# Kernel tuning notes

Hardware: AMD Instinct MI355X
Metric: run time of the kernel (lower is better)

## Reference

```python
import jax, jax.numpy as jnp
import numpy as np

N_HEADS = 16
D_HEAD = 64
THETA = 10000.0


def _rope_tables(S, dh, dtype):
    inv_freq = 1.0 / (THETA ** (jnp.arange(0, dh, 2, dtype=jnp.float32) / dh))  # [dh/2]
    ang = jnp.arange(S, dtype=jnp.float32)[:, None] * inv_freq[None, :]  # [S, dh/2]
    return jnp.cos(ang).astype(dtype), jnp.sin(ang).astype(dtype)


def _apply_rope(t, cos, sin):
    # t: [B,S,H,dh]; interleaved complex pairs (even=real, odd=imag)
    B, S, H, dh = t.shape
    tr = t.reshape(B, S, H, dh // 2, 2)
    a, b = tr[..., 0], tr[..., 1]
    c = cos[None, :, None, :]
    s = sin[None, :, None, :]
    ra = a * c - b * s
    rb = a * s + b * c
    return jnp.stack([ra, rb], axis=-1).reshape(B, S, H, dh)


def setup_inputs() -> dict:
    key = jax.random.key(0)
    ks = jax.random.split(key, 5)
    B, S, D = 2, 2048, 1024
    x = jax.random.normal(ks[0], (B, S, D), dtype=jnp.float32)
    scale = 1.0 / np.sqrt(D)
    wq = jax.random.normal(ks[1], (D, D), dtype=jnp.float32) * scale
    wk = jax.random.normal(ks[2], (D, D), dtype=jnp.float32) * scale
    wv = jax.random.normal(ks[3], (D, D), dtype=jnp.float32) * scale
    wo = jax.random.normal(ks[4], (D, D), dtype=jnp.float32) * scale
    return {"x": x, "wq": wq, "wk": wk, "wv": wv, "wo": wo}


def reference(x, wq, wk, wv, wo):
    B, S, D = x.shape
    H, dh = N_HEADS, D_HEAD
    q = (x @ wq).reshape(B, S, H, dh)
    k = (x @ wk).reshape(B, S, H, dh)
    v = (x @ wv).reshape(B, S, H, dh)
    cos, sin = _rope_tables(S, dh, x.dtype)
    q = _apply_rope(q, cos, sin)
    k = _apply_rope(k, cos, sin)
    # [B,H,S,S] scores
    scale = 1.0 / np.sqrt(dh).astype(np.float32)
    attn = jnp.einsum('bqhd,bkhd->bhqk', q, k) * scale
    causal = jnp.tril(jnp.ones((S, S), dtype=bool))[None, None]
    attn = jnp.where(causal, attn, -jnp.inf)
    probs = jax.nn.softmax(attn, axis=-1)
    head_out = jnp.einsum('bhqk,bkhd->bqhd', probs, v).reshape(B, S, D)
    return head_out @ wo
```

## Files before the change

kernel.cpp:

```cpp
#include <hip/hip_runtime.h>
#include <hip/hip_bf16.h>

#define S_LEN   2048
#define BATCH   2
#define NH      16
#define DH      64
#define DMODEL  1024
#define MTOT    (BATCH * S_LEN)

typedef __attribute__((ext_vector_type(4))) float f32x4;
typedef __attribute__((ext_vector_type(8))) short s16x8;
typedef __attribute__((ext_vector_type(4))) short s16x4;

#define MFMA_BF16(a, b, c) __builtin_amdgcn_mfma_f32_16x16x32_bf16((a), (b), (c), 0, 0, 0)

static __device__ __forceinline__ short f2bf(float f) {
    union { float f; unsigned u; } v; v.f = f;
    unsigned r = v.u + 0x7fffu + ((v.u >> 16) & 1u);
    return (short)(r >> 16);
}

static __device__ __forceinline__ unsigned cvtpk_bf16(float lo, float hi) {
    unsigned r;
    asm volatile("v_cvt_pk_bf16_f32 %0, %1, %2" : "=v"(r) : "v"(lo), "v"(hi));
    return r;
}

static __device__ __forceinline__ void gload_lds16(const void* g, void* l) {
    __builtin_amdgcn_global_load_lds(
        (const __attribute__((address_space(1))) void*)g,
        (__attribute__((address_space(3))) void*)l, 16, 0, 0);
}

#define VM_WAIT(N) asm volatile("s_waitcnt vmcnt(" #N ")" ::: "memory")

static __device__ __forceinline__ void barrier_sync() {
    asm volatile("" ::: "memory");
    __builtin_amdgcn_s_barrier();
    asm volatile("" ::: "memory");
}

__global__ __launch_bounds__(256) void prep_all(const float* __restrict__ wq,
                                                const float* __restrict__ wk,
                                                const float* __restrict__ wv,
                                                const float* __restrict__ wo,
                                                const float* __restrict__ x,
                                                short* __restrict__ wtb,
                                                short* __restrict__ xb,
                                                float* __restrict__ cosT,
                                                float* __restrict__ sinT) {
    const int t = threadIdx.x;
    if (blockIdx.z < 4) {
        const float* W = (blockIdx.z == 0) ? wq : (blockIdx.z == 1) ? wk
                       : (blockIdx.z == 2) ? wv : wo;
        short* out = wtb + (size_t)blockIdx.z * DMODEL * DMODEL;

        __shared__ short T[64][72];
        const int k0 = blockIdx.y * 64, n0 = blockIdx.x * 64;

        #pragma unroll
        for (int p = 0; p < 4; ++p) {
            const int kk = p * 16 + (t >> 4);
            const int nn = (t & 15) * 4;
            f32x4 v = *(const f32x4*)(W + (size_t)(k0 + kk) * DMODEL + n0 + nn);
            #pragma unroll
            for (int j = 0; j < 4; ++j) T[nn + j][kk] = f2bf(v[j]);
        }
        __syncthreads();
        #pragma unroll
        for (int p = 0; p < 4; ++p) {
            const int nn = p * 16 + (t >> 4);
            const int kk = (t & 15) * 4;
            *(s16x4*)(out + (size_t)(n0 + nn) * DMODEL + k0 + kk) = *(const s16x4*)&T[nn][kk];
        }
    } else {
        const int slice = blockIdx.z - 4;
        const int blk = blockIdx.y * 16 + blockIdx.x;
        const size_t tb = ((size_t)(slice * 256 + blk) * 256 + t) * 16;
        #pragma unroll
        for (int jj = 0; jj < 2; ++jj) {
            const size_t i = tb + jj * 8;
            f32x4 a = *(const f32x4*)(x + i);
            f32x4 b = *(const f32x4*)(x + i + 4);
            s16x8 o;
            #pragma unroll
            for (int j = 0; j < 4; ++j) { o[j] = f2bf(a[j]); o[4 + j] = f2bf(b[j]); }
            *(s16x8*)(xb + i) = o;
        }
        if (slice == 0) {
            const int idx = blk * 256 + t;
            const int s = idx >> 5, ii = idx & 31;
            const float inv = exp2f(-(float)ii * (13.287712379549449f / 32.0f));
            const float ang = (float)s * inv;
            cosT[idx] = cosf(ang);
            sinT[idx] = sinf(ang);
        }
    }
}

__device__ __forceinline__ void gemm_tile(const short* __restrict__ A,
                                          const short* __restrict__ Bt,
                                          int m0, int n0, short* SM,
                                          f32x4 acc[4][4]) {
    const int tid  = threadIdx.x;
    const int lane = tid & 63;
    const int wv   = tid >> 6;
    const int wm   = (wv >> 1) * 64;
    const int wn   = (wv & 1) * 64;
    const int g = lane >> 4, c16 = lane & 15;

    short* Asb = SM;
    short* Bsb = SM + 12288;

    const int srow = tid >> 2;
    const int schk = (tid & 3) ^ ((tid >> 3) & 3);
    const short* ga0 = A  + (size_t)(m0 + srow)      * DMODEL + schk * 8;
    const short* ga1 = A  + (size_t)(m0 + 64 + srow) * DMODEL + schk * 8;
    const short* gb0 = Bt + (size_t)(n0 + srow)      * DMODEL + schk * 8;
    const short* gb1 = Bt + (size_t)(n0 + 64 + srow) * DMODEL + schk * 8;
    const int lw = wv * 512;

    #define STAGE_G(buf, ko) do { \
        gload_lds16(ga0 + (ko), Asb + (buf) * 4096 + lw); \
        gload_lds16(ga1 + (ko), Asb + (buf) * 4096 + 2048 + lw); \
        gload_lds16(gb0 + (ko), Bsb + (buf) * 4096 + lw); \
        gload_lds16(gb1 + (ko), Bsb + (buf) * 4096 + 2048 + lw); \
    } while (0)

    STAGE_G(0, 0);
    STAGE_G(1, 32);

    const int rlo = (g ^ ((c16 >> 1) & 3)) << 3;
    for (int ks = 0; ks < 32; ++ks) {
        if (ks < 31) { VM_WAIT(4); } else { VM_WAIT(0); }
        barrier_sync();
        if (ks + 2 < 32) STAGE_G((ks + 2) % 3, (ks + 2) * 32);
        const int cur = ks % 3;
        s16x8 af[4], bfr[4];
        #pragma unroll
        for (int i = 0; i < 4; ++i)
            af[i] = *(const s16x8*)&Asb[cur * 4096 + (wm + i * 16 + c16) * 32 + rlo];
        #pragma unroll
        for (int j = 0; j < 4; ++j)
            bfr[j] = *(const s16x8*)&Bsb[cur * 4096 + (wn + j * 16 + c16) * 32 + rlo];
        #pragma unroll
        for (int i = 0; i < 4; ++i)
            #pragma unroll
            for (int j = 0; j < 4; ++j)
                acc[i][j] = MFMA_BF16(af[i], bfr[j], acc[i][j]);
    }
    #undef STAGE_G
}

__device__ __forceinline__ void gemm_tile64(const short* __restrict__ A,
                                            const short* __restrict__ Bt,
                                            int m0, int n0, short* SM,
                                            f32x4 acc[4][2]) {
    const int tid  = threadIdx.x;
    const int lane = tid & 63;
    const int wv   = tid >> 6;
    const int wm   = (wv >> 1) * 64;
    const int wn   = (wv & 1) * 32;
    const int g = lane >> 4, c16 = lane & 15;

    short* Asb = SM;
    short* Bsb = SM + 12288;

    const int srow = tid >> 2;
    const int schk = (tid & 3) ^ ((tid >> 3) & 3);
    const short* ga0 = A  + (size_t)(m0 + srow)      * DMODEL + schk * 8;
    const short* ga1 = A  + (size_t)(m0 + 64 + srow) * DMODEL + schk * 8;
    const short* gb0 = Bt + (size_t)(n0 + srow)      * DMODEL + schk * 8;
    const int lw = wv * 512;

    #define SG64(buf, ko) do { \
        gload_lds16(ga0 + (ko), Asb + (buf) * 4096 + lw); \
        gload_lds16(ga1 + (ko), Asb + (buf) * 4096 + 2048 + lw); \
        gload_lds16(gb0 + (ko), Bsb + (buf) * 2048 + lw); \
    } while (0)

    SG64(0, 0);
    SG64(1, 32);

    const int rlo = (g ^ ((c16 >> 1) & 3)) << 3;
    for (int ks = 0; ks < 32; ++ks) {
        if (ks < 31) { VM_WAIT(3); } else { VM_WAIT(0); }
        barrier_sync();
        if (ks + 2 < 32) SG64((ks + 2) % 3, (ks + 2) * 32);
        const int cur = ks % 3;
        s16x8 af[4], bfr[2];
        #pragma unroll
        for (int i = 0; i < 4; ++i)
            af[i] = *(const s16x8*)&Asb[cur * 4096 + (wm + i * 16 + c16) * 32 + rlo];
        #pragma unroll
        for (int j = 0; j < 2; ++j)
            bfr[j] = *(const s16x8*)&Bsb[cur * 2048 + (wn + j * 16 + c16) * 32 + rlo];
        #pragma unroll
        for (int i = 0; i < 4; ++i)
            #pragma unroll
            for (int j = 0; j < 2; ++j)
                acc[i][j] = MFMA_BF16(af[i], bfr[j], acc[i][j]);
    }
    #undef SG64
}

__global__ __launch_bounds__(256) void gemm_qkv(const short* __restrict__ xb,
                                                const short* __restrict__ wtb,
                                                short* __restrict__ Qo,
                                                short* __restrict__ Ko,
                                                short* __restrict__ Vt,
                                                const float* __restrict__ cosT,
                                                const float* __restrict__ sinT) {
    __shared__ __align__(16) short SM[24576];

    const int dd    = blockIdx.x + 24 * blockIdx.y;
    const int xcd   = dd & 7;
    const int local = dd >> 3;
    const int ty = (xcd & 3) * 8 + local / 12;
    const int tx = (xcd >> 2) * 12 + local % 12;
    const int m0 = ty * 128, n0 = tx * 128;
    const int z  = tx >> 3;

    f32x4 acc[4][4] = {};
    gemm_tile(xb, wtb, m0, n0, SM, acc);

    const int tid  = threadIdx.x;
    const int lane = tid & 63;
    const int wv   = tid >> 6;
    const int wm   = (wv >> 1) * 64, wn = (wv & 1) * 64;
    const int g = lane >> 4, c16 = lane & 15;
    const int hbase = (n0 & 1023) >> 6;

    barrier_sync();
    short (*RP)[136] = (short(*)[136])SM;

    if (z < 2) {
        short* outp = (z == 0) ? Qo : Ko;
        const float post = (z == 0) ? 0.18033688011112042f : 1.0f;
        #pragma unroll
        for (int j = 0; j < 4; ++j) {
            const int nl = wn + j * 16 + c16;
            const int d  = (n0 + nl) & 63;
            #pragma unroll
            for (int i = 0; i < 4; ++i) {
                #pragma unroll
                for (int r = 0; r < 4; ++r) {
                    const int ml = wm + i * 16 + g * 4 + r;
                    const int s  = (m0 + ml) & (S_LEN - 1);
                    float v = acc[i][j][r];
                    float vo = __shfl_xor(v, 1, 64);
                    float cs = cosT[s * 32 + (d >> 1)];
                    float sn = sinT[s * 32 + (d >> 1)];
                    float res = (d & 1) ? (vo * sn + v * cs) : (v * cs - vo * sn);
                    RP[ml][nl] = f2bf(res * post);
                }
            }
        }
        barrier_sync();
        #pragma unroll
        for (int pass = 0; pass < 8; ++pass) {
            const int row = pass * 32 + (tid >> 3);
            const int k   = tid & 7;
            const int hh = row >> 7, ss = row & 127;
            const int m = m0 + ss;
            const int s = m & (S_LEN - 1), b = m >> 11;
            short* dst = outp + (((size_t)b * NH + hbase + hh) * S_LEN + s) * DH + k * 8;
            *(s16x8*)dst = *(const s16x8*)&RP[ss][hh * 64 + k * 8];
        }
    } else {
        #pragma unroll
        for (int j = 0; j < 4; ++j) {
            const int nl = wn + j * 16 + c16;
            #pragma unroll
            for (int i = 0; i < 4; ++i) {
                const int mlb = wm + i * 16 + g * 4;
                s16x4 pk;
                #pragma unroll
                for (int r = 0; r < 4; ++r) pk[r] = f2bf(acc[i][j][r]);
                *(s16x4*)&RP[nl][mlb] = pk;
            }
        }
        barrier_sync();
        const int b = m0 >> 11, sr0 = m0 & (S_LEN - 1);
        #pragma unroll
        for (int pass = 0; pass < 8; ++pass) {
            const int row = pass * 16 + (tid >> 4);
            const int k   = tid & 15;
            const int h = hbase + (row >> 6), d = row & 63;
            short* dst = Vt + (((size_t)b * NH + h) * DH + d) * S_LEN + sr0 + k * 8;
            *(s16x8*)dst = *(const s16x8*)&RP[row][k * 8];
        }
    }
}

__global__ __launch_bounds__(256) void attn(const short* __restrict__ Q,
                                            const short* __restrict__ K,
                                            const short* __restrict__ Vt,
                                            short* __restrict__ O) {
    const int tid  = threadIdx.x;
    const int lane = tid & 63;
    const int w    = tid >> 6;
    const int g = lane >> 4, c16 = lane & 15;
    const int bh = blockIdx.x;
    const int ci = 31 - blockIdx.y;
    const int ntiles = ci + 1;
    const int wq0 = ci * 64 + w * 16;
    const size_t base = (size_t)bh * S_LEN * DH;
    const short* Kb = K + base;
    const short* Vb = Vt + (size_t)bh * DH * S_LEN;
    const int b = bh >> 4, h = bh & 15;

    __shared__ __align__(16) short KL[2][4096];
    __shared__ __align__(16) short VL[2][4096];
    __shared__ __align__(16) short P2[4][16][72];

    const int kr = tid >> 3;
    const int kc = (tid & 7) ^ (kr & 7);
    const short* kg0 = Kb + (size_t)kr * DH + (kc << 3);
    const short* kg1 = Kb + (size_t)(32 + kr) * DH + (kc << 3);
    const short* vg0 = Vb + (size_t)kr * S_LEN + (kc << 3);
    const short* vg1 = Vb + (size_t)(32 + kr) * S_LEN + (kc << 3);
    const int lw = w * 512;
    const int kx = c16 & 7;

    gload_lds16(kg0, &KL[0][lw]);
    gload_lds16(kg1, &KL[0][2048 + lw]);
    gload_lds16(vg0, &VL[0][lw]);
    gload_lds16(vg1, &VL[0][2048 + lw]);
    s16x8 bq0 = *(const s16x8*)(Q + base + (size_t)(wq0 + c16) * DH + g * 8);
    s16x8 bq1 = *(const s16x8*)(Q + base + (size_t)(wq0 + c16) * DH + 32 + g * 8);
    VM_WAIT(0);
    barrier_sync();

    f32x4 o[4] = {};
    float lsum = 0.f;

    for (int tt = 0; tt < ntiles; ++tt) {
        const int cur = tt & 1;
        const bool more = (tt + 1 < ntiles);
        if (more) {
            const size_t ko = (size_t)(tt + 1) * 64;
            gload_lds16(kg0 + ko * DH, &KL[cur ^ 1][lw]);
            gload_lds16(kg1 + ko * DH, &KL[cur ^ 1][2048 + lw]);
            gload_lds16(vg0 + ko,      &VL[cur ^ 1][lw]);
            gload_lds16(vg1 + ko,      &VL[cur ^ 1][2048 + lw]);
        }

        f32x4 s[4];
        __builtin_amdgcn_s_setprio(1);
        #pragma unroll
        for (int cg = 0; cg < 4; ++cg) {
            const int krow = (cg * 16 + c16) * 64;
            s16x8 kf0 = *(const s16x8*)&KL[cur][krow + ((g ^ kx) << 3)];
            s16x8 kf1 = *(const s16x8*)&KL[cur][krow + (((4 + g) ^ kx) << 3)];
            f32x4 zz = {};
            zz = MFMA_BF16(kf0, bq0, zz);
            s[cg] = MFMA_BF16(kf1, bq1, zz);
        }
        __builtin_amdgcn_s_setprio(0);

        s16x8 vf[4][2];
        #pragma unroll
        for (int nt = 0; nt < 4; ++nt) {
            const int vr = (nt * 16 + c16) * 64;
            vf[nt][0] = *(const s16x8*)&VL[cur][vr + ((g ^ kx) << 3)];
            vf[nt][1] = *(const s16x8*)&VL[cur][vr + (((4 + g) ^ kx) << 3)];
        }

        const bool diag = (tt == ci);
        const int qrel = w * 16 + c16;
        #pragma unroll
        for (int cg = 0; cg < 4; ++cg) {
            float e[4];
            #pragma unroll
            for (int r = 0; r < 4; ++r) {
                e[r] = exp2f(s[cg][r]);
                if (diag && (cg * 16 + g * 4 + r > qrel)) e[r] = 0.f;
            }
            lsum += (e[0] + e[1]) + (e[2] + e[3]);
            uint2 pk;
            pk.x = cvtpk_bf16(e[0], e[1]);
            pk.y = cvtpk_bf16(e[2], e[3]);
            *(uint2*)&P2[w][c16][cg * 16 + g * 4] = pk;
        }
        asm volatile("s_waitcnt lgkmcnt(0)" ::: "memory");
        s16x8 ap0 = *(const s16x8*)&P2[w][c16][g * 8];
        s16x8 ap1 = *(const s16x8*)&P2[w][c16][32 + g * 8];

        __builtin_amdgcn_s_setprio(1);
        #pragma unroll
        for (int nt = 0; nt < 4; ++nt) {
            o[nt] = MFMA_BF16(ap0, vf[nt][0], o[nt]);
            o[nt] = MFMA_BF16(ap1, vf[nt][1], o[nt]);
        }
        __builtin_amdgcn_s_setprio(0);

        if (more) { VM_WAIT(0); }
        barrier_sync();
    }

    float lt = lsum;
    lt += __shfl_xor(lt, 16, 64);
    lt += __shfl_xor(lt, 32, 64);
    #pragma unroll
    for (int r = 0; r < 4; ++r) {
        const float linv = 1.0f / __shfl(lt, g * 4 + r, 64);
        #pragma unroll
        for (int nt = 0; nt < 4; ++nt) {
            O[((size_t)(b * S_LEN + wq0 + g * 4 + r)) * DMODEL
              + h * DH + nt * 16 + c16] = f2bf(o[nt][r] * linv);
        }
    }
}

__global__ __launch_bounds__(256) void gemm_o(const short* __restrict__ Ob,
                                              const short* __restrict__ WoT,
                                              float* __restrict__ C) {
    __shared__ __align__(16) short SMl[18432];

    const int dd = blockIdx.x + 16 * blockIdx.y;
    const int ti = (dd & 7) * 64 + (dd >> 3);
    const int tx = ti & 15, ty = ti >> 4;
    const int m0 = ty * 128, n0 = tx * 64;

    f32x4 acc[4][2] = {};
    gemm_tile64(Ob, WoT, m0, n0, SMl, acc);

    const int tid  = threadIdx.x;
    const int lane = tid & 63;
    const int wv   = tid >> 6;
    const int wm   = (wv >> 1) * 64, wn = (wv & 1) * 32;
    const int g = lane >> 4, c16 = lane & 15;

    #pragma unroll
    for (int i = 0; i < 4; ++i)
        #pragma unroll
        for (int j = 0; j < 2; ++j) {
            const int n = n0 + wn + j * 16 + c16;
            #pragma unroll
            for (int r = 0; r < 4; ++r) {
                const int m = m0 + wm + i * 16 + g * 4 + r;
                C[(size_t)m * DMODEL + n] = acc[i][j][r];
            }
        }
}

extern "C" void kernel_launch(void* const* d_in, const int* in_sizes, int n_in,
                              void* d_out, int out_size, void* d_ws, size_t ws_size,
                              hipStream_t stream) {
    const float* x  = (const float*)d_in[0];
    const float* wq = (const float*)d_in[1];
    const float* wk = (const float*)d_in[2];
    const float* wv = (const float*)d_in[3];
    const float* wo = (const float*)d_in[4];
    float* out = (float*)d_out;

    char* ws = (char*)d_ws;
    short* wtb  = (short*)ws;
    short* xb   = (short*)(ws + (8ull  << 20));
    float* cosT = (float*)(ws + (16ull << 20));
    float* sinT = (float*)(ws + (16ull << 20) + (256ull << 10));
    short* Qb   = (short*)(ws + (17ull << 20));
    short* Kb   = (short*)(ws + (25ull << 20));
    short* Vtb  = (short*)(ws + (33ull << 20));
    short* Ob   = (short*)(ws + (41ull << 20));

    prep_all<<<dim3(16, 16, 8), 256, 0, stream>>>(wq, wk, wv, wo, x,
                                                  wtb, xb, cosT, sinT);

    gemm_qkv<<<dim3(24, 32), 256, 0, stream>>>(xb, wtb, Qb, Kb, Vtb, cosT, sinT);
    attn    <<<dim3(32, 32), 256, 0, stream>>>(Qb, Kb, Vtb, Ob);
    gemm_o  <<<dim3(16, 32), 256, 0, stream>>>(Ob, wtb + 3ull * DMODEL * DMODEL, out);
}
```

Baseline: 109.3 us.

## Enlarge QKV GEMM tile to 256x128 with double-buffered LDS pipeline

The QKV projection GEMM moves from 128x128 to 256x128 output tiles, so each wave holds an 8x4 MFMA accumulator block and the grid is halved to 384 blocks. The three-stage LDS ring with partial vmcnt waits becomes a two-stage double buffer that waits for all loads and barriers at the end of each k-step. The RoPE and V-transpose epilogue is split into two 128-row passes that reuse the same LDS staging buffer. The aim is more operand reuse per loaded byte and fewer blocks. The cost is doubled accumulator registers, lower occupancy, a shallower pipeline with full waits, and fewer blocks per CU.

```diff
diff --git a/kernel.cpp b/kernel.cpp
--- a/kernel.cpp
+++ b/kernel.cpp
@@ -98,58 +98,59 @@
     }
 }
 
-__device__ __forceinline__ void gemm_tile(const short* __restrict__ A,
-                                          const short* __restrict__ Bt,
-                                          int m0, int n0, short* SM,
-                                          f32x4 acc[4][4]) {
+__device__ __forceinline__ void gemm_tile256(const short* __restrict__ A,
+                                             const short* __restrict__ Bt,
+                                             int m0, int n0, short* SM,
+                                             f32x4 acc[8][4]) {
     const int tid  = threadIdx.x;
     const int lane = tid & 63;
     const int wv   = tid >> 6;
-    const int wm   = (wv >> 1) * 64;
+    const int wm   = (wv >> 1) * 128;
     const int wn   = (wv & 1) * 64;
     const int g = lane >> 4, c16 = lane & 15;
 
     short* Asb = SM;
-    short* Bsb = SM + 12288;
+    short* Bsb = SM + 16384;
 
     const int srow = tid >> 2;
     const int schk = (tid & 3) ^ ((tid >> 3) & 3);
-    const short* ga0 = A  + (size_t)(m0 + srow)      * DMODEL + schk * 8;
-    const short* ga1 = A  + (size_t)(m0 + 64 + srow) * DMODEL + schk * 8;
-    const short* gb0 = Bt + (size_t)(n0 + srow)      * DMODEL + schk * 8;
-    const short* gb1 = Bt + (size_t)(n0 + 64 + srow) * DMODEL + schk * 8;
+    const short* gA = A  + (size_t)(m0 + srow) * DMODEL + schk * 8;
+    const short* gB = Bt + (size_t)(n0 + srow) * DMODEL + schk * 8;
     const int lw = wv * 512;
 
-    #define STAGE_G(buf, ko) do { \
-        gload_lds16(ga0 + (ko), Asb + (buf) * 4096 + lw); \
-        gload_lds16(ga1 + (ko), Asb + (buf) * 4096 + 2048 + lw); \
-        gload_lds16(gb0 + (ko), Bsb + (buf) * 4096 + lw); \
-        gload_lds16(gb1 + (ko), Bsb + (buf) * 4096 + 2048 + lw); \
+    #define STG(buf, ko) do { \
+        gload_lds16(gA + (ko),                       Asb + (buf) * 8192 + lw); \
+        gload_lds16(gA + (size_t) 64 * DMODEL + (ko), Asb + (buf) * 8192 + 2048 + lw); \
+        gload_lds16(gA + (size_t)128 * DMODEL + (ko), Asb + (buf) * 8192 + 4096 + lw); \
+        gload_lds16(gA + (size_t)192 * DMODEL + (ko), Asb + (buf) * 8192 + 6144 + lw); \
+        gload_lds16(gB + (ko),                       Bsb + (buf) * 4096 + lw); \
+        gload_lds16(gB + (size_t) 64 * DMODEL + (ko), Bsb + (buf) * 4096 + 2048 + lw); \
     } while (0)
 
-    STAGE_G(0, 0);
-    STAGE_G(1, 32);
+    STG(0, 0);
+    VM_WAIT(0);
+    barrier_sync();
 
     const int rlo = (g ^ ((c16 >> 1) & 3)) << 3;
     for (int ks = 0; ks < 32; ++ks) {
-        if (ks < 31) { VM_WAIT(4); } else { VM_WAIT(0); }
-        barrier_sync();
-        if (ks + 2 < 32) STAGE_G((ks + 2) % 3, (ks + 2) * 32);
-        const int cur = ks % 3;
-        s16x8 af[4], bfr[4];
-        #pragma unroll
-        for (int i = 0; i < 4; ++i)
-            af[i] = *(const s16x8*)&Asb[cur * 4096 + (wm + i * 16 + c16) * 32 + rlo];
+        const int cur = ks & 1;
+        if (ks + 1 < 32) STG(cur ^ 1, (ks + 1) * 32);
+        s16x8 af[8], bfr[4];
+        #pragma unroll
+        for (int i = 0; i < 8; ++i)
+            af[i] = *(const s16x8*)&Asb[cur * 8192 + (wm + i * 16 + c16) * 32 + rlo];
         #pragma unroll
         for (int j = 0; j < 4; ++j)
             bfr[j] = *(const s16x8*)&Bsb[cur * 4096 + (wn + j * 16 + c16) * 32 + rlo];
         #pragma unroll
-        for (int i = 0; i < 4; ++i)
+        for (int i = 0; i < 8; ++i)
             #pragma unroll
             for (int j = 0; j < 4; ++j)
                 acc[i][j] = MFMA_BF16(af[i], bfr[j], acc[i][j]);
-    }
-    #undef STAGE_G
+        asm volatile("s_waitcnt vmcnt(0) lgkmcnt(0)" ::: "memory");
+        barrier_sync();
+    }
+    #undef STG
 }
 
 __device__ __forceinline__ void gemm_tile64(const short* __restrict__ A,
@@ -204,91 +205,104 @@
     #undef SG64
 }
 
-__global__ __launch_bounds__(256) void gemm_qkv(const short* __restrict__ xb,
-                                                const short* __restrict__ wtb,
-                                                short* __restrict__ Qo,
-                                                short* __restrict__ Ko,
-                                                short* __restrict__ Vt,
-                                                const float* __restrict__ cosT,
-                                                const float* __restrict__ sinT) {
+__global__ __launch_bounds__(256, 2) void gemm_qkv(const short* __restrict__ xb,
+                                                   const short* __restrict__ wtb,
+                                                   short* __restrict__ Qo,
+                                                   short* __restrict__ Ko,
+                                                   short* __restrict__ Vt,
+                                                   const float* __restrict__ cosT,
+                                                   const float* __restrict__ sinT) {
     __shared__ __align__(16) short SM[24576];
 
     const int dd    = blockIdx.x + 24 * blockIdx.y;
     const int xcd   = dd & 7;
     const int local = dd >> 3;
-    const int ty = (xcd & 3) * 8 + local / 12;
+    const int ty = (xcd & 3) * 4 + local / 12;
     const int tx = (xcd >> 2) * 12 + local % 12;
-    const int m0 = ty * 128, n0 = tx * 128;
+    const int m0 = ty * 256, n0 = tx * 128;
     const int z  = tx >> 3;
 
-    f32x4 acc[4][4] = {};
-    gemm_tile(xb, wtb, m0, n0, SM, acc);
+    f32x4 acc[8][4] = {};
+    gemm_tile256(xb, wtb, m0, n0, SM, acc);
 
     const int tid  = threadIdx.x;
     const int lane = tid & 63;
     const int wv   = tid >> 6;
-    const int wm   = (wv >> 1) * 64, wn = (wv & 1) * 64;
+    const int wp   = wv >> 1;
+    const int wn   = (wv & 1) * 64;
     const int g = lane >> 4, c16 = lane & 15;
     const int hbase = (n0 & 1023) >> 6;
 
-    barrier_sync();
     short (*RP)[136] = (short(*)[136])SM;
 
     if (z < 2) {
         short* outp = (z == 0) ? Qo : Ko;
         const float post = (z == 0) ? 0.18033688011112042f : 1.0f;
-        #pragma unroll
-        for (int j = 0; j < 4; ++j) {
-            const int nl = wn + j * 16 + c16;
-            const int d  = (n0 + nl) & 63;
-            #pragma unroll
-            for (int i = 0; i < 4; ++i) {
+        #pragma unroll 1
+        for (int p2 = 0; p2 < 2; ++p2) {
+            if (wp == p2) {
                 #pragma unroll
-                for (int r = 0; r < 4; ++r) {
-                    const int ml = wm + i * 16 + g * 4 + r;
-                    const int s  = (m0 + ml) & (S_LEN - 1);
-                    float v = acc[i][j][r];
-                    float vo = __shfl_xor(v, 1, 64);
-                    float cs = cosT[s * 32 + (d >> 1)];
-                    float sn = sinT[s * 32 + (d >> 1)];
-                    float res = (d & 1) ? (vo * sn + v * cs) : (v * cs - vo * sn);
-                    RP[ml][nl] = f2bf(res * post);
+                for (int j = 0; j < 4; ++j) {
+                    const int nl = wn + j * 16 + c16;
+                    const int d  = (n0 + nl) & 63;
+                    #pragma unroll
+                    for (int i = 0; i < 8; ++i) {
+                        #pragma unroll
+                        for (int r = 0; r < 4; ++r) {
+                            const int ml = i * 16 + g * 4 + r;
+                            const int s  = (m0 + p2 * 128 + ml) & (S_LEN - 1);
+                            float v = acc[i][j][r];
+                            float vo = __shfl_xor(v, 1, 64);
+                            float cs = cosT[s * 32 + (d >> 1)];
+                            float sn = sinT[s * 32 + (d >> 1)];
+                            float res = (d & 1) ? (vo * sn + v * cs) : (v * cs - vo * sn);
+                            RP[ml][nl] = f2bf(res * post);
+                        }
+                    }
                 }
             }
-        }
-        barrier_sync();
-        #pragma unroll
-        for (int pass = 0; pass < 8; ++pass) {
-            const int row = pass * 32 + (tid >> 3);
-            const int k   = tid & 7;
-            const int hh = row >> 7, ss = row & 127;
-            const int m = m0 + ss;
-            const int s = m & (S_LEN - 1), b = m >> 11;
-            short* dst = outp + (((size_t)b * NH + hbase + hh) * S_LEN + s) * DH + k * 8;
-            *(s16x8*)dst = *(const s16x8*)&RP[ss][hh * 64 + k * 8];
+            barrier_sync();
+            #pragma unroll
+            for (int pass = 0; pass < 8; ++pass) {
+                const int row = pass * 32 + (tid >> 3);
+                const int k   = tid & 7;
+                const int hh = row >> 7, ss = row & 127;
+                const int m = m0 + p2 * 128 + ss;
+                const int s = m & (S_LEN - 1), b = m >> 11;
+                short* dst = outp + (((size_t)b * NH + hbase + hh) * S_LEN + s) * DH + k * 8;
+                *(s16x8*)dst = *(const s16x8*)&RP[ss][hh * 64 + k * 8];
+            }
+            barrier_sync();
         }
     } else {
-        #pragma unroll
-        for (int j = 0; j < 4; ++j) {
-            const int nl = wn + j * 16 + c16;
-            #pragma unroll
-            for (int i = 0; i < 4; ++i) {
-                const int mlb = wm + i * 16 + g * 4;
-                s16x4 pk;
+        #pragma unroll 1
+        for (int p2 = 0; p2 < 2; ++p2) {
+            if (wp == p2) {
                 #pragma unroll
-                for (int r = 0; r < 4; ++r) pk[r] = f2bf(acc[i][j][r]);
-                *(s16x4*)&RP[nl][mlb] = pk;
-            }
-        }
-        barrier_sync();
-        const int b = m0 >> 11, sr0 = m0 & (S_LEN - 1);
-        #pragma unroll
-        for (int pass = 0; pass < 8; ++pass) {
-            const int row = pass * 16 + (tid >> 4);
-            const int k   = tid & 15;
-            const int h = hbase + (row >> 6), d = row & 63;
-            short* dst = Vt + (((size_t)b * NH + h) * DH + d) * S_LEN + sr0 + k * 8;
-            *(s16x8*)dst = *(const s16x8*)&RP[row][k * 8];
+                for (int j = 0; j < 4; ++j) {
+                    const int nl = wn + j * 16 + c16;
+                    #pragma unroll
+                    for (int i = 0; i < 8; ++i) {
+                        const int mlb = i * 16 + g * 4;
+                        s16x4 pk;
+                        #pragma unroll
+                        for (int r = 0; r < 4; ++r) pk[r] = f2bf(acc[i][j][r]);
+                        *(s16x4*)&RP[nl][mlb] = pk;
+                    }
+                }
+            }
+            barrier_sync();
+            const int mb = m0 + p2 * 128;
+            const int b = mb >> 11, sr0 = mb & (S_LEN - 1);
+            #pragma unroll
+            for (int pass = 0; pass < 8; ++pass) {
+                const int row = pass * 16 + (tid >> 4);
+                const int k   = tid & 15;
+                const int h = hbase + (row >> 6), d = row & 63;
+                short* dst = Vt + (((size_t)b * NH + h) * DH + d) * S_LEN + sr0 + k * 8;
+                *(s16x8*)dst = *(const s16x8*)&RP[row][k * 8];
+            }
+            barrier_sync();
         }
     }
 }
@@ -468,7 +482,7 @@
     prep_all<<<dim3(16, 16, 8), 256, 0, stream>>>(wq, wk, wv, wo, x,
                                                   wtb, xb, cosT, sinT);
 
-    gemm_qkv<<<dim3(24, 32), 256, 0, stream>>>(xb, wtb, Qb, Kb, Vtb, cosT, sinT);
+    gemm_qkv<<<dim3(24, 16), 256, 0, stream>>>(xb, wtb, Qb, Kb, Vtb, cosT, sinT);
     attn    <<<dim3(32, 32), 256, 0, stream>>>(Qb, Kb, Vtb, Ob);
     gemm_o  <<<dim3(16, 32), 256, 0, stream>>>(Ob, wtb + 3ull * DMODEL * DMODEL, out);
 }
```

New measurement: 286.1 us. +161.7%, slower.

## Enlarge attention query tile to 128 rows with two query groups per wave

Applied to the files above, without the earlier changes.

The attention kernel now gives each block 128 query rows instead of 64, and each wave handles 32 rows as two 16-row groups. Every K/V tile loaded into LDS and every set of K/V fragments read from it is therefore reused across twice as many queries, roughly halving K/V traffic per query. The grid is halved and block indices are remapped so that long-causal and short-causal blocks are interleaved for balance across CUs. Waves skip tiles past their own diagonal, which leaves some waves idle near the end of each block and raises register pressure from the doubled accumulators.

```diff
diff --git a/kernel.cpp b/kernel.cpp
--- a/kernel.cpp
+++ b/kernel.cpp
@@ -301,10 +301,14 @@
     const int lane = tid & 63;
     const int w    = tid >> 6;
     const int g = lane >> 4, c16 = lane & 15;
-    const int bh = blockIdx.x;
-    const int ci = 31 - blockIdx.y;
-    const int ntiles = ci + 1;
-    const int wq0 = ci * 64 + w * 16;
+
+    const int d_ = blockIdx.x + 32 * blockIdx.y;
+    int ci, bh;
+    if (d_ < 256) { ci = 15 - (d_ & 15); bh = d_ >> 4; }
+    else          { const int j = d_ - 256; ci = j & 15; bh = 16 + (j >> 4); }
+    const int ntiles = 2 * ci + 2;
+    const int tw = 2 * ci + (w >> 1);
+    const int wq0 = ci * 128 + w * 32;
     const size_t base = (size_t)bh * S_LEN * DH;
     const short* Kb = K + base;
     const short* Vb = Vt + (size_t)bh * DH * S_LEN;
@@ -312,7 +316,7 @@
 
     __shared__ __align__(16) short KL[2][4096];
     __shared__ __align__(16) short VL[2][4096];
-    __shared__ __align__(16) short P2[4][16][72];
+    __shared__ __align__(16) short P2[4][32][72];
 
     const int kr = tid >> 3;
     const int kc = (tid & 7) ^ (kr & 7);
@@ -327,13 +331,18 @@
     gload_lds16(kg1, &KL[0][2048 + lw]);
     gload_lds16(vg0, &VL[0][lw]);
     gload_lds16(vg1, &VL[0][2048 + lw]);
-    s16x8 bq0 = *(const s16x8*)(Q + base + (size_t)(wq0 + c16) * DH + g * 8);
-    s16x8 bq1 = *(const s16x8*)(Q + base + (size_t)(wq0 + c16) * DH + 32 + g * 8);
+    s16x8 bq[2][2];
+    #pragma unroll
+    for (int qg = 0; qg < 2; ++qg) {
+        const short* qp = Q + base + (size_t)(wq0 + qg * 16 + c16) * DH;
+        bq[qg][0] = *(const s16x8*)(qp + g * 8);
+        bq[qg][1] = *(const s16x8*)(qp + 32 + g * 8);
+    }
     VM_WAIT(0);
     barrier_sync();
 
-    f32x4 o[4] = {};
-    float lsum = 0.f;
+    f32x4 o[2][4] = {};
+    float lsum[2] = {};
 
     for (int tt = 0; tt < ntiles; ++tt) {
         const int cur = tt & 1;
@@ -346,69 +355,88 @@
             gload_lds16(vg1 + ko,      &VL[cur ^ 1][2048 + lw]);
         }
 
-        f32x4 s[4];
-        __builtin_amdgcn_s_setprio(1);
-        #pragma unroll
-        for (int cg = 0; cg < 4; ++cg) {
-            const int krow = (cg * 16 + c16) * 64;
-            s16x8 kf0 = *(const s16x8*)&KL[cur][krow + ((g ^ kx) << 3)];
-            s16x8 kf1 = *(const s16x8*)&KL[cur][krow + (((4 + g) ^ kx) << 3)];
-            f32x4 zz = {};
-            zz = MFMA_BF16(kf0, bq0, zz);
-            s[cg] = MFMA_BF16(kf1, bq1, zz);
-        }
-        __builtin_amdgcn_s_setprio(0);
-
-        s16x8 vf[4][2];
-        #pragma unroll
-        for (int nt = 0; nt < 4; ++nt) {
-            const int vr = (nt * 16 + c16) * 64;
-            vf[nt][0] = *(const s16x8*)&VL[cur][vr + ((g ^ kx) << 3)];
-            vf[nt][1] = *(const s16x8*)&VL[cur][vr + (((4 + g) ^ kx) << 3)];
-        }
-
-        const bool diag = (tt == ci);
-        const int qrel = w * 16 + c16;
-        #pragma unroll
-        for (int cg = 0; cg < 4; ++cg) {
-            float e[4];
-            #pragma unroll
-            for (int r = 0; r < 4; ++r) {
-                e[r] = exp2f(s[cg][r]);
-                if (diag && (cg * 16 + g * 4 + r > qrel)) e[r] = 0.f;
-            }
-            lsum += (e[0] + e[1]) + (e[2] + e[3]);
-            uint2 pk;
-            pk.x = cvtpk_bf16(e[0], e[1]);
-            pk.y = cvtpk_bf16(e[2], e[3]);
-            *(uint2*)&P2[w][c16][cg * 16 + g * 4] = pk;
-        }
-        asm volatile("s_waitcnt lgkmcnt(0)" ::: "memory");
-        s16x8 ap0 = *(const s16x8*)&P2[w][c16][g * 8];
-        s16x8 ap1 = *(const s16x8*)&P2[w][c16][32 + g * 8];
-
-        __builtin_amdgcn_s_setprio(1);
-        #pragma unroll
-        for (int nt = 0; nt < 4; ++nt) {
-            o[nt] = MFMA_BF16(ap0, vf[nt][0], o[nt]);
-            o[nt] = MFMA_BF16(ap1, vf[nt][1], o[nt]);
-        }
-        __builtin_amdgcn_s_setprio(0);
+        if (tt <= tw) {
+            s16x8 kf[4][2];
+            #pragma unroll
+            for (int cg = 0; cg < 4; ++cg) {
+                const int krow = (cg * 16 + c16) * 64;
+                kf[cg][0] = *(const s16x8*)&KL[cur][krow + ((g ^ kx) << 3)];
+                kf[cg][1] = *(const s16x8*)&KL[cur][krow + (((4 + g) ^ kx) << 3)];
+            }
+            f32x4 s[2][4];
+            __builtin_amdgcn_s_setprio(1);
+            #pragma unroll
+            for (int qg = 0; qg < 2; ++qg)
+                #pragma unroll
+                for (int cg = 0; cg < 4; ++cg) {
+                    f32x4 zz = {};
+                    zz = MFMA_BF16(kf[cg][0], bq[qg][0], zz);
+                    s[qg][cg] = MFMA_BF16(kf[cg][1], bq[qg][1], zz);
+                }
+            __builtin_amdgcn_s_setprio(0);
+
+            s16x8 vf[4][2];
+            #pragma unroll
+            for (int nt = 0; nt < 4; ++nt) {
+                const int vr = (nt * 16 + c16) * 64;
+                vf[nt][0] = *(const s16x8*)&VL[cur][vr + ((g ^ kx) << 3)];
+                vf[nt][1] = *(const s16x8*)&VL[cur][vr + (((4 + g) ^ kx) << 3)];
+            }
+
+            const bool diag = (tt == tw);
+            #pragma unroll
+            for (int qg = 0; qg < 2; ++qg) {
+                const int qrel = (w & 1) * 32 + qg * 16 + c16;
+                #pragma unroll
+                for (int cg = 0; cg < 4; ++cg) {
+                    float e[4];
+                    #pragma unroll
+                    for (int r = 0; r < 4; ++r) {
+                        e[r] = exp2f(s[qg][cg][r]);
+                        if (diag && (cg * 16 + g * 4 + r > qrel)) e[r] = 0.f;
+                    }
+                    lsum[qg] += (e[0] + e[1]) + (e[2] + e[3]);
+                    uint2 pk;
+                    pk.x = cvtpk_bf16(e[0], e[1]);
+                    pk.y = cvtpk_bf16(e[2], e[3]);
+                    *(uint2*)&P2[w][qg * 16 + c16][cg * 16 + g * 4] = pk;
+                }
+            }
+            asm volatile("s_waitcnt lgkmcnt(0)" ::: "memory");
+            s16x8 ap[2][2];
+            #pragma unroll
+            for (int qg = 0; qg < 2; ++qg) {
+                ap[qg][0] = *(const s16x8*)&P2[w][qg * 16 + c16][g * 8];
+                ap[qg][1] = *(const s16x8*)&P2[w][qg * 16 + c16][32 + g * 8];
+            }
+            __builtin_amdgcn_s_setprio(1);
+            #pragma unroll
+            for (int qg = 0; qg < 2; ++qg)
+                #pragma unroll
+                for (int nt = 0; nt < 4; ++nt) {
+                    o[qg][nt] = MFMA_BF16(ap[qg][0], vf[nt][0], o[qg][nt]);
+                    o[qg][nt] = MFMA_BF16(ap[qg][1], vf[nt][1], o[qg][nt]);
+                }
+            __builtin_amdgcn_s_setprio(0);
+        }
 
         if (more) { VM_WAIT(0); }
         barrier_sync();
     }
 
-    float lt = lsum;
-    lt += __shfl_xor(lt, 16, 64);
-    lt += __shfl_xor(lt, 32, 64);
     #pragma unroll
-    for (int r = 0; r < 4; ++r) {
-        const float linv = 1.0f / __shfl(lt, g * 4 + r, 64);
-        #pragma unroll
-        for (int nt = 0; nt < 4; ++nt) {
-            O[((size_t)(b * S_LEN + wq0 + g * 4 + r)) * DMODEL
-              + h * DH + nt * 16 + c16] = f2bf(o[nt][r] * linv);
+    for (int qg = 0; qg < 2; ++qg) {
+        float lt = lsum[qg];
+        lt += __shfl_xor(lt, 16, 64);
+        lt += __shfl_xor(lt, 32, 64);
+        #pragma unroll
+        for (int r = 0; r < 4; ++r) {
+            const float linv = 1.0f / __shfl(lt, g * 4 + r, 64);
+            #pragma unroll
+            for (int nt = 0; nt < 4; ++nt) {
+                O[((size_t)(b * S_LEN + wq0 + qg * 16 + g * 4 + r)) * DMODEL
+                  + h * DH + nt * 16 + c16] = f2bf(o[qg][nt][r] * linv);
+            }
         }
     }
 }
@@ -469,6 +497,6 @@
                                                   wtb, xb, cosT, sinT);
 
     gemm_qkv<<<dim3(24, 32), 256, 0, stream>>>(xb, wtb, Qb, Kb, Vtb, cosT, sinT);
-    attn    <<<dim3(32, 32), 256, 0, stream>>>(Qb, Kb, Vtb, Ob);
+    attn    <<<dim3(32, 16), 256, 0, stream>>>(Qb, Kb, Vtb, Ob);
     gemm_o  <<<dim3(16, 32), 256, 0, stream>>>(Ob, wtb + 3ull * DMODEL * DMODEL, out);
 }
```

After: 125.0 us. 14.4% more time.
